# Optimization experiments

Measured on AMD Instinct MI355X. Metric: run time of the kernel, lower is better.

## Reference

```python
import jax, jax.numpy as jnp
import numpy as np

SCALES = (1, 3, 6)
PRECISION = 10  # pywt default: 2**10 samples of psi on [-5, 5]


def _gaus1_filters():
    """Replicates pywt.cwt's integrated-wavelet filters for wavelet='gaus1'.

    pywt: psi, x = wavelet.wavefun(10); int_psi = cumsum(psi)*step; per scale a:
    j = arange(a*(x[-1]-x[0])+1)/(a*step) -> int indices; filter = int_psi[j][::-1];
    conv = np.convolve(data, filter). np.convolve flips its kernel, so the
    equivalent cross-correlation kernel (lax.conv semantics) is int_psi[j].
    """
    x = np.linspace(-5.0, 5.0, 2 ** PRECISION)
    step = x[1] - x[0]
    psi = -2.0 * x * np.exp(-x ** 2) / (np.pi / 2.0) ** 0.25
    int_psi = np.cumsum(psi) * step
    filts = []
    for a in SCALES:
        j = (np.arange(a * (x[-1] - x[0]) + 1) / (a * step)).astype(np.int64)
        j = j[j < int_psi.size]
        filts.append(int_psi[j].astype(np.float32))  # correlation kernel
    return filts

_FILTS = _gaus1_filters()


def setup_inputs() -> dict:
    key = jax.random.key(0)
    x = jax.random.normal(key, (32, 4096, 64), dtype=jnp.float32)
    return {"x": x}


def reference(x):
    B, S, C = x.shape
    sig = jnp.transpose(x, (0, 2, 1)).reshape(B * C, 1, S)  # [B*C, 1, S]
    outs = []
    for a, f in zip(SCALES, _FILTS):
        L = f.shape[0]
        k = jnp.asarray(f).reshape(1, 1, L)
        # full convolution (np.convolve): pad L-1 both sides
        conv = jax.lax.conv_general_dilated(
            sig, k, window_strides=(1,), padding=[(L - 1, L - 1)],
            dimension_numbers=("NCH", "OIH", "NCH"))  # [B*C, 1, S+L-1]
        coef = -np.sqrt(a).astype(np.float32) * jnp.diff(conv, axis=-1)  # [B*C,1,S+L-2]
        d = (coef.shape[-1] - S) / 2.0
        coef = coef[..., int(np.floor(d)): coef.shape[-1] - int(np.ceil(d))]  # [B*C,1,S]
        outs.append(coef)
    out = jnp.concatenate(outs, axis=1).reshape(B, C, len(SCALES), S)
    return jnp.transpose(out, (0, 2, 3, 1))  # [B, 3, S, C]
```

## Files before the change

kernel.cpp:

```cpp
#include <hip/hip_runtime.h>
#include <math.h>

#define S_LEN  4096
#define NCH    64
#define TILE_S 128
#define RPT    16
#define TY     8
#define HALO_L 31
#define STAGE  (TILE_S + 61)
#define WLEN   77
#define PRE    20

struct WtArgs { float w6[62]; float w3[32]; float w1[12]; };


template <int T, int R>
struct FmaR {
  static __device__ __forceinline__ void run(const WtArgs& W, const float (&win)[WLEN],
                                             float (&a6)[RPT], float (&a3)[RPT],
                                             float (&a1)[RPT]) {
    a6[R] = fmaf(W.w6[T], win[T + R], a6[R]);
    if constexpr (T >= 15 && T <= 46) a3[R] = fmaf(W.w3[T - 15], win[T + R], a3[R]);
    if constexpr (T >= 25 && T <= 36) a1[R] = fmaf(W.w1[T - 25], win[T + R], a1[R]);
    FmaR<T, R + 1>::run(W, win, a6, a3, a1);
  }
};
template <int T>
struct FmaR<T, RPT> {
  static __device__ __forceinline__ void run(const WtArgs&, const float (&)[WLEN],
                                             float (&)[RPT], float (&)[RPT], float (&)[RPT]) {}
};

template <int T>
struct Step {
  static __device__ __forceinline__ void run(const float* __restrict__ col, const WtArgs& W,
                                             float (&win)[WLEN], float (&a6)[RPT],
                                             float (&a3)[RPT], float (&a1)[RPT]) {
    if constexpr (T + PRE < WLEN) win[T + PRE] = col[(T + PRE) * NCH];
    FmaR<T, 0>::run(W, win, a6, a3, a1);
    Step<T + 1>::run(col, W, win, a6, a3, a1);
  }
};
template <>
struct Step<62> {
  static __device__ __forceinline__ void run(const float* __restrict__, const WtArgs&,
                                             float (&)[WLEN], float (&)[RPT],
                                             float (&)[RPT], float (&)[RPT]) {}
};

template <int K>
struct Pre {
  static __device__ __forceinline__ void run(const float* __restrict__ col, float (&win)[WLEN]) {
    win[K] = col[K * NCH];
    Pre<K + 1>::run(col, win);
  }
};
template <>
struct Pre<PRE> {
  static __device__ __forceinline__ void run(const float* __restrict__, float (&)[WLEN]) {}
};

template <int R>
struct Store {
  static __device__ __forceinline__ void run(float* __restrict__ o1, float* __restrict__ o3,
                                             float* __restrict__ o6, const float (&a6)[RPT],
                                             const float (&a3)[RPT], const float (&a1)[RPT]) {
    o1[(size_t)R * NCH] = a1[R];
    o3[(size_t)R * NCH] = a3[R];
    o6[(size_t)R * NCH] = a6[R];
    Store<R + 1>::run(o1, o3, o6, a6, a3, a1);
  }
};
template <>
struct Store<RPT> {
  static __device__ __forceinline__ void run(float* __restrict__, float* __restrict__,
                                             float* __restrict__, const float (&)[RPT],
                                             const float (&)[RPT], const float (&)[RPT]) {}
};

template <int R>
struct Zero {
  static __device__ __forceinline__ void run(float (&a6)[RPT], float (&a3)[RPT], float (&a1)[RPT]) {
    a6[R] = 0.f; a3[R] = 0.f; a1[R] = 0.f;
    Zero<R + 1>::run(a6, a3, a1);
  }
};
template <>
struct Zero<RPT> {
  static __device__ __forceinline__ void run(float (&)[RPT], float (&)[RPT], float (&)[RPT]) {}
};

__global__ __launch_bounds__(512, 4)
void cwt_main(const float* __restrict__ x, float* __restrict__ out, const WtArgs W) {
  __shared__ __align__(16) float lds[STAGE * NCH];

  const int c   = threadIdx.x;
  const int ty  = threadIdx.y;
  const int tid = ty * 64 + c;
  const int b   = blockIdx.y;
  const int s0  = blockIdx.x * TILE_S;
  const float* xb = x + (size_t)b * S_LEN * NCH;
  const int row0 = s0 - HALO_L;

  float4 stg[6];
  #pragma unroll
  for (int i = 0; i < 6; ++i) {
    const int idx = tid + i * 512;
    const int r = idx >> 4, q = idx & 15;
    const int row = row0 + r;
    float4 v = make_float4(0.f, 0.f, 0.f, 0.f);
    if (idx < STAGE * 16 && row >= 0 && row < S_LEN)
      v = *(const float4*)(xb + ((size_t)row * NCH + (q << 2)));
    stg[i] = v;
  }
  #pragma unroll
  for (int i = 0; i < 6; ++i) {
    const int idx = tid + i * 512;
    if (idx < STAGE * 16)
      *(float4*)(&lds[(idx >> 4) * NCH + ((idx & 15) << 2)]) = stg[i];
  }
  __syncthreads();

  const int base = ty * RPT;
  const float* col = &lds[base * NCH + c];

  float win[WLEN];
  float a6[RPT], a3[RPT], a1[RPT];
  Zero<0>::run(a6, a3, a1);
  Pre<0>::run(col, win);
  Step<0>::run(col, W, win, a6, a3, a1);

  const int srow = s0 + base;
  float* o1 = out + (((size_t)b * 3 + 0) * S_LEN + srow) * NCH + c;
  float* o3 = out + (((size_t)b * 3 + 1) * S_LEN + srow) * NCH + c;
  float* o6 = out + (((size_t)b * 3 + 2) * S_LEN + srow) * NCH + c;
  Store<0>::run(o1, o3, o6, a6, a3, a1);
}

extern "C" void kernel_launch(void* const* d_in, const int* in_sizes, int n_in,
                              void* d_out, int out_size, void* d_ws, size_t ws_size,
                              hipStream_t stream) {
  (void)n_in; (void)out_size; (void)d_ws; (void)ws_size;
  const float* x = (const float*)d_in[0];
  float* out = (float*)d_out;
  const int B = in_sizes[0] / (S_LEN * NCH);

  WtArgs W;
  {
    static double ip[1024];
    const double delta = 10.0 / 1023.0;
    const double step  = (-5.0 + delta) + 5.0;
    const double cn    = pow(3.141592653589793 * 0.5, 0.25);
    double s = 0.0;
    for (int i = 0; i < 1024; ++i) {
      const double xi  = (i == 1023) ? 5.0 : ((double)i * delta - 5.0);
      const double psi = (-2.0 * xi) * exp(-(xi * xi)) / cn;
      s += psi;
      ip[i] = s * step;
    }
    const int   as_[3] = {6, 3, 1};
    const int   lf_[3] = {61, 31, 11};
    float*      wp_[3] = {W.w6, W.w3, W.w1};
    for (int si = 0; si < 3; ++si) {
      const double denom = (double)as_[si] * step;
      const float  sqa   = (float)sqrt((double)as_[si]);
      const int    lf    = lf_[si];
      for (int t = 0; t <= lf; ++t) {
        float km1 = 0.f, kt = 0.f;
        if (t >= 1)      km1 = (float)ip[(long)(((double)(t - 1)) / denom)];
        if (t <= lf - 1) kt  = (float)ip[(long)(((double)t) / denom)];
        wp_[si][t] = -sqa * (km1 - kt);
      }
    }
  }

  dim3 grid(S_LEN / TILE_S, B);
  dim3 block(NCH, TY);
  hipLaunchKernelGGL(cwt_main, grid, block, 0, stream, x, out, W);
}
```

Baseline: 134.7 us.

## Drop LDS staging and read input windows directly from global memory

Removes the shared-memory tile and its barrier. Each thread now loads its 77-row sliding window straight from global memory, using a branch-free interior path and a bounds-checked edge path for the first and last strips. The block shrinks to 256 threads and the grid grows to match. This removes LDS writes and the sync, but each strip now re-reads overlapping halo rows from global memory and relies on the L2/L1 caches for reuse.

New measurement: 143.3 us. +6.4%, slower.

```diff
diff --git a/kernel.cpp b/kernel.cpp
--- a/kernel.cpp
+++ b/kernel.cpp
@@ -3,11 +3,8 @@
 
 #define S_LEN  4096
 #define NCH    64
-#define TILE_S 128
 #define RPT    16
-#define TY     8
-#define HALO_L 31
-#define STAGE  (TILE_S + 61)
+#define TY     4
 #define WLEN   77
 #define PRE    20
 
@@ -31,33 +28,45 @@
                                              float (&)[RPT], float (&)[RPT], float (&)[RPT]) {}
 };
 
-template <int T>
+template <int K, bool EDGE>
+static __device__ __forceinline__ float ldw(const float* __restrict__ col, int rowbase) {
+  if constexpr (EDGE) {
+    const int row = rowbase + K;
+    return (row >= 0 && row < S_LEN) ? col[K * NCH] : 0.f;
+  } else {
+    return col[K * NCH];
+  }
+}
+
+template <int T, bool EDGE>
 struct Step {
-  static __device__ __forceinline__ void run(const float* __restrict__ col, const WtArgs& W,
-                                             float (&win)[WLEN], float (&a6)[RPT],
-                                             float (&a3)[RPT], float (&a1)[RPT]) {
-    if constexpr (T + PRE < WLEN) win[T + PRE] = col[(T + PRE) * NCH];
+  static __device__ __forceinline__ void run(const float* __restrict__ col, int rowbase,
+                                             const WtArgs& W, float (&win)[WLEN],
+                                             float (&a6)[RPT], float (&a3)[RPT],
+                                             float (&a1)[RPT]) {
+    if constexpr (T + PRE < WLEN) win[T + PRE] = ldw<T + PRE, EDGE>(col, rowbase);
     FmaR<T, 0>::run(W, win, a6, a3, a1);
-    Step<T + 1>::run(col, W, win, a6, a3, a1);
+    Step<T + 1, EDGE>::run(col, rowbase, W, win, a6, a3, a1);
   }
 };
-template <>
-struct Step<62> {
-  static __device__ __forceinline__ void run(const float* __restrict__, const WtArgs&,
+template <bool EDGE>
+struct Step<62, EDGE> {
+  static __device__ __forceinline__ void run(const float* __restrict__, int, const WtArgs&,
                                              float (&)[WLEN], float (&)[RPT],
                                              float (&)[RPT], float (&)[RPT]) {}
 };
 
-template <int K>
+template <int K, bool EDGE>
 struct Pre {
-  static __device__ __forceinline__ void run(const float* __restrict__ col, float (&win)[WLEN]) {
-    win[K] = col[K * NCH];
-    Pre<K + 1>::run(col, win);
+  static __device__ __forceinline__ void run(const float* __restrict__ col, int rowbase,
+                                             float (&win)[WLEN]) {
+    win[K] = ldw<K, EDGE>(col, rowbase);
+    Pre<K + 1, EDGE>::run(col, rowbase, win);
   }
 };
-template <>
-struct Pre<PRE> {
-  static __device__ __forceinline__ void run(const float* __restrict__, float (&)[WLEN]) {}
+template <bool EDGE>
+struct Pre<PRE, EDGE> {
+  static __device__ __forceinline__ void run(const float* __restrict__, int, float (&)[WLEN]) {}
 };
 
 template <int R>
@@ -90,50 +99,32 @@
   static __device__ __forceinline__ void run(float (&)[RPT], float (&)[RPT], float (&)[RPT]) {}
 };
 
-__global__ __launch_bounds__(512, 4)
+__global__ __launch_bounds__(256, 4)
 void cwt_main(const float* __restrict__ x, float* __restrict__ out, const WtArgs W) {
-  __shared__ __align__(16) float lds[STAGE * NCH];
+  const int c     = threadIdx.x;
+  const int ty    = threadIdx.y;
+  const int b     = blockIdx.y;
+  const int strip = blockIdx.x * TY + ty;
+  const int s0w   = strip * RPT;
+  const int rowbase = s0w - 31;
 
-  const int c   = threadIdx.x;
-  const int ty  = threadIdx.y;
-  const int tid = ty * 64 + c;
-  const int b   = blockIdx.y;
-  const int s0  = blockIdx.x * TILE_S;
-  const float* xb = x + (size_t)b * S_LEN * NCH;
-  const int row0 = s0 - HALO_L;
-
-  float4 stg[6];
-  #pragma unroll
-  for (int i = 0; i < 6; ++i) {
-    const int idx = tid + i * 512;
-    const int r = idx >> 4, q = idx & 15;
-    const int row = row0 + r;
-    float4 v = make_float4(0.f, 0.f, 0.f, 0.f);
-    if (idx < STAGE * 16 && row >= 0 && row < S_LEN)
-      v = *(const float4*)(xb + ((size_t)row * NCH + (q << 2)));
-    stg[i] = v;
-  }
-  #pragma unroll
-  for (int i = 0; i < 6; ++i) {
-    const int idx = tid + i * 512;
-    if (idx < STAGE * 16)
-      *(float4*)(&lds[(idx >> 4) * NCH + ((idx & 15) << 2)]) = stg[i];
-  }
-  __syncthreads();
-
-  const int base = ty * RPT;
-  const float* col = &lds[base * NCH + c];
+  const float* col = x + (size_t)b * S_LEN * NCH + (ptrdiff_t)rowbase * NCH + c;
 
   float win[WLEN];
   float a6[RPT], a3[RPT], a1[RPT];
   Zero<0>::run(a6, a3, a1);
-  Pre<0>::run(col, win);
-  Step<0>::run(col, W, win, a6, a3, a1);
 
-  const int srow = s0 + base;
-  float* o1 = out + (((size_t)b * 3 + 0) * S_LEN + srow) * NCH + c;
-  float* o3 = out + (((size_t)b * 3 + 1) * S_LEN + srow) * NCH + c;
-  float* o6 = out + (((size_t)b * 3 + 2) * S_LEN + srow) * NCH + c;
+  if (strip >= 2 && strip <= 253) {
+    Pre<0, false>::run(col, rowbase, win);
+    Step<0, false>::run(col, rowbase, W, win, a6, a3, a1);
+  } else {
+    Pre<0, true>::run(col, rowbase, win);
+    Step<0, true>::run(col, rowbase, W, win, a6, a3, a1);
+  }
+
+  float* o1 = out + (((size_t)b * 3 + 0) * S_LEN + s0w) * NCH + c;
+  float* o3 = out + (((size_t)b * 3 + 1) * S_LEN + s0w) * NCH + c;
+  float* o6 = out + (((size_t)b * 3 + 2) * S_LEN + s0w) * NCH + c;
   Store<0>::run(o1, o3, o6, a6, a3, a1);
 }
 
@@ -174,7 +165,7 @@
     }
   }
 
-  dim3 grid(S_LEN / TILE_S, B);
+  dim3 grid(256 / TY, B);
   dim3 block(NCH, TY);
   hipLaunchKernelGGL(cwt_main, grid, block, 0, stream, x, out, W);
 }
```
